# Kernel tuning notes

Measured on AMD Instinct MI355X. Metric: run time of the kernel, lower is better.

## Reference

```python
import jax, jax.numpy as jnp
import numpy as np

D_IN = 1024
N_HEADS = 16
DEPTH = D_IN // N_HEADS
SCALE = float(np.sqrt(DEPTH))


def setup_inputs() -> dict:
    key = jax.random.key(0)
    ks = jax.random.split(key, 11)
    B, S = 4, 1024
    s = 0.02
    return {
        "q": jax.random.normal(ks[0], (B, S, D_IN), jnp.float32),
        "k": jax.random.normal(ks[1], (B, S, D_IN), jnp.float32),
        "v": jax.random.normal(ks[2], (B, S, D_IN), jnp.float32),
        "mask": jnp.zeros((1, 1, S, S), jnp.float32),
        "wq_w": jax.random.normal(ks[3], (D_IN, D_IN), jnp.float32) * s,
        "wq_b": jax.random.normal(ks[4], (D_IN,), jnp.float32) * s,
        "wk_w": jax.random.normal(ks[5], (D_IN, D_IN), jnp.float32) * s,
        "wk_b": jax.random.normal(ks[6], (D_IN,), jnp.float32) * s,
        "wv_w": jax.random.normal(ks[7], (D_IN, D_IN), jnp.float32) * s,
        "wv_b": jax.random.normal(ks[8], (D_IN,), jnp.float32) * s,
        "pl_w": jax.random.normal(ks[9], (D_IN, D_IN), jnp.float32) * s,
        "pl_b": jax.random.normal(ks[10], (D_IN,), jnp.float32) * s,
    }


def _split_heads(x):
    # [B, S, D] -> [B, H, S, depth]
    B, S, _ = x.shape
    return x.reshape(B, S, N_HEADS, DEPTH).transpose(0, 2, 1, 3)


def reference(q, k, v, mask, wq_w, wq_b, wk_w, wk_b, wv_w, wv_b, pl_w, pl_b):
    # torch Linear: y = x @ W.T + b
    qh = _split_heads(q @ wq_w.T + wq_b)
    kh = _split_heads(k @ wk_w.T + wk_b)
    vh = _split_heads(v @ wv_w.T + wv_b)
    # [B, H, Sq, Sk]
    logits = jnp.einsum("bhqd,bhkd->bhqk", qh, kh) / SCALE
    logits = logits + mask * (-1e9)
    weights = jax.nn.softmax(logits, axis=-1)
    attn = jnp.einsum("bhqk,bhkd->bhqd", weights, vh)
    B = q.shape[0]
    attn = attn.transpose(0, 2, 1, 3).reshape(B, -1, D_IN)
    return attn @ pl_w.T + pl_b
```

## Files before the change

kernel.cpp:

```cpp
#include <hip/hip_runtime.h>
#include <stdint.h>

#define B_ 4
#define S_ 1024
#define DMODEL 1024
#define H_ 16
#define DP_ 64

typedef __attribute__((ext_vector_type(8))) short short8;
typedef __attribute__((ext_vector_type(4))) float floatx4;
typedef __attribute__((ext_vector_type(8))) unsigned short ushort8;
typedef __attribute__((ext_vector_type(4))) unsigned short ushort4v;

#define LOG2E 1.44269504088896f

__device__ __forceinline__ unsigned short f2bf(float x) {
    union { float f; unsigned int u; } c; c.f = x;
    unsigned int r = c.u + 0x7FFFu + ((c.u >> 16) & 1u);
    return (unsigned short)(r >> 16);
}
__device__ __forceinline__ unsigned short f2bf_fast(float x) {
    union { float f; unsigned int u; } c; c.f = x;
    return (unsigned short)((c.u + 0x8000u) >> 16);
}
__device__ __forceinline__ float bf2f(unsigned short b) {
    union { float f; unsigned int u; } c; c.u = ((unsigned int)b) << 16;
    return c.f;
}

#if __has_builtin(__builtin_amdgcn_exp2f)
#define EXP2(x) __builtin_amdgcn_exp2f(x)
#else
#define EXP2(x) exp2f(x)
#endif

#define GLDS16(gp, lp) __builtin_amdgcn_global_load_lds( \
    (const __attribute__((address_space(1))) void*)(gp),  \
    (__attribute__((address_space(3))) void*)(lp), 16, 0, 0)

__global__ __launch_bounds__(256) void convert_all(
    const float* __restrict__ q, const float* __restrict__ k, const float* __restrict__ v,
    const float* __restrict__ wq, const float* __restrict__ wk, const float* __restrict__ wv,
    const float* __restrict__ wp, const float* __restrict__ mask,
    unsigned short* __restrict__ ws)
{
    const unsigned g = blockIdx.x * 256u + threadIdx.x;
    const float* s; unsigned short* d; unsigned off; float sc = 1.0f;
    if (g < 524288u)        { s = q;  d = ws;            off = g; }
    else if (g < 1048576u)  { s = k;  d = ws + 4194304;  off = g - 524288u; }
    else if (g < 1572864u)  { s = v;  d = ws + 8388608;  off = g - 1048576u; }
    else if (g < 1703936u)  { s = wq; d = ws + 12582912; off = g - 1572864u; }
    else if (g < 1835008u)  { s = wk; d = ws + 13631488; off = g - 1703936u; }
    else if (g < 1966080u)  { s = wv; d = ws + 14680064; off = g - 1835008u; }
    else if (g < 2097152u)  { s = wp; d = ws + 15728640; off = g - 1966080u; }
    else { s = mask; d = ws + 16777216; off = g - 2097152u; sc = -1e9f * LOG2E; }
    const floatx4 a = ((const floatx4*)s)[(size_t)off * 2];
    const floatx4 b = ((const floatx4*)s)[(size_t)off * 2 + 1];
    ushort8 r;
    r[0] = f2bf(a[0] * sc); r[1] = f2bf(a[1] * sc); r[2] = f2bf(a[2] * sc); r[3] = f2bf(a[3] * sc);
    r[4] = f2bf(b[0] * sc); r[5] = f2bf(b[1] * sc); r[6] = f2bf(b[2] * sc); r[7] = f2bf(b[3] * sc);
    ((ushort8*)d)[off] = r;
}

template<bool SWAP>
__device__ __forceinline__ void gemm_body(
    const unsigned short* __restrict__ X, const unsigned short* __restrict__ W,
    const int row0, const int col0,
    unsigned short* Xs, unsigned short* Ws, floatx4* acc)
{
    const int tid = threadIdx.x, w = tid >> 6, lane = tid & 63;
    const int l15 = lane & 15, l4 = lane >> 4;
    const int wr = w >> 1, wc = w & 1;
    const int srow = lane >> 3;
    const int sgrp = (lane & 7) ^ srow;
    auto* XsL = (__attribute__((address_space(3))) unsigned short*)Xs;
    auto* WsL = (__attribute__((address_space(3))) unsigned short*)Ws;

    for (int it = 0; it < 16; it++) {
        const int kk = it * 64;
        __syncthreads();
        for (int j = 0; j < 4; j++) {
            const int rb = w * 32 + j * 8;
            GLDS16(X + (size_t)(row0 + rb + srow) * DMODEL + kk + sgrp * 8, XsL + rb * 64);
            GLDS16(W + (size_t)(col0 + rb + srow) * DMODEL + kk + sgrp * 8, WsL + rb * 64);
        }
        __syncthreads();
        for (int ks = 0; ks < 2; ks++) {
            const int slot = ((ks * 4 + l4) ^ (l15 & 7)) * 8;
            short8 xf[4], wf[4];
            for (int t = 0; t < 4; t++) {
                xf[t] = *(const short8*)(Xs + (wr * 64 + t * 16 + l15) * 64 + slot);
                wf[t] = *(const short8*)(Ws + (wc * 64 + t * 16 + l15) * 64 + slot);
            }
            for (int a = 0; a < 4; a++)
                for (int b2 = 0; b2 < 4; b2++)
                    acc[a * 4 + b2] = SWAP
                        ? __builtin_amdgcn_mfma_f32_16x16x32_bf16(wf[a], xf[b2], acc[a * 4 + b2], 0, 0, 0)
                        : __builtin_amdgcn_mfma_f32_16x16x32_bf16(xf[a], wf[b2], acc[a * 4 + b2], 0, 0, 0);
        }
    }
}

__global__ __launch_bounds__(256, 3) void qkv_gemm(
    const unsigned short* __restrict__ Xall, const unsigned short* __restrict__ Wall,
    const float* __restrict__ bq, const float* __restrict__ bk, const float* __restrict__ bv,
    unsigned short* __restrict__ Qh, unsigned short* __restrict__ Kh,
    unsigned short* __restrict__ Vt)
{
    __shared__ unsigned short Xs[8192];
    __shared__ unsigned short Ws[8192];
    const int sel = blockIdx.y >> 5;
    const int row0 = (blockIdx.y & 31) * 128, col0 = blockIdx.x * 128;
    const unsigned short* X = Xall + (size_t)sel * 4194304;
    const unsigned short* W = Wall + (size_t)sel * 1048576;
    const float* bias = (sel == 0) ? bq : (sel == 1) ? bk : bv;

    const int tid = threadIdx.x, w = tid >> 6, lane = tid & 63;
    const int l15 = lane & 15, l4 = lane >> 4;
    const int wr = w >> 1, wc = w & 1;

    floatx4 acc[16];
    for (int i = 0; i < 16; i++) acc[i] = (floatx4){0.f, 0.f, 0.f, 0.f};

    if (sel < 2) {
        gemm_body<true>(X, W, row0, col0, Xs, Ws, acc);
        unsigned short* Out = sel ? Kh : Qh;
        const float scale = sel ? 1.0f : 0.125f * LOG2E;
        for (int nt = 0; nt < 4; nt++) {
            const int n0 = col0 + wc * 64 + nt * 16 + l4 * 4;
            const floatx4 bv4 = *(const floatx4*)(bias + n0);
            const int h = n0 >> 6, d0 = n0 & 63;
            for (int mt = 0; mt < 4; mt++) {
                const int m = row0 + wr * 64 + mt * 16 + l15;
                const int b = m >> 10, s = m & 1023;
                const floatx4 a = acc[nt * 4 + mt];
                ushort4v pk;
                for (int i = 0; i < 4; i++) pk[i] = f2bf((a[i] + bv4[i]) * scale);
                *(ushort4v*)(Out + (((size_t)(b * H_ + h) * S_ + s) * DP_ + d0)) = pk;
            }
        }
    } else {
        gemm_body<false>(X, W, row0, col0, Xs, Ws, acc);
        for (int mt = 0; mt < 4; mt++) {
            const int m0 = row0 + wr * 64 + mt * 16 + l4 * 4;
            const int b = m0 >> 10, s0 = m0 & 1023;
            for (int nt = 0; nt < 4; nt++) {
                const int n = col0 + wc * 64 + nt * 16 + l15;
                const int h = n >> 6, d = n & 63;
                const float bvv = bias[n];
                const floatx4 a = acc[mt * 4 + nt];
                ushort4v pk;
                for (int i = 0; i < 4; i++) pk[i] = f2bf(a[i] + bvv);
                *(ushort4v*)(Vt + (((size_t)(b * H_ + h) * DP_ + d) * S_ + s0)) = pk;
            }
        }
    }
}

__global__ __launch_bounds__(256, 4) void out_gemm(
    const unsigned short* __restrict__ X, const unsigned short* __restrict__ W,
    const float* __restrict__ bias, float* __restrict__ Out)
{
    __shared__ unsigned short Xs[128 * 64];
    __shared__ unsigned short Ws[64 * 64];
    const int row0 = blockIdx.y * 128, col0 = blockIdx.x * 64;
    const int tid = threadIdx.x, w = tid >> 6, lane = tid & 63;
    const int l15 = lane & 15, l4 = lane >> 4;
    const int srow = lane >> 3, sgrp = (lane & 7) ^ srow;
    auto* XsL = (__attribute__((address_space(3))) unsigned short*)Xs;
    auto* WsL = (__attribute__((address_space(3))) unsigned short*)Ws;

    floatx4 acc[8];
    for (int i = 0; i < 8; i++) acc[i] = (floatx4){0.f, 0.f, 0.f, 0.f};

    for (int it = 0; it < 16; it++) {
        const int kk = it * 64;
        __syncthreads();
        for (int j = 0; j < 4; j++) {
            const int rb = w * 32 + j * 8;
            GLDS16(X + (size_t)(row0 + rb + srow) * DMODEL + kk + sgrp * 8, XsL + rb * 64);
        }
        for (int j = 0; j < 2; j++) {
            const int rb = w * 16 + j * 8;
            GLDS16(W + (size_t)(col0 + rb + srow) * DMODEL + kk + sgrp * 8, WsL + rb * 64);
        }
        __syncthreads();
        for (int ks = 0; ks < 2; ks++) {
            const int slot = ((ks * 4 + l4) ^ (l15 & 7)) * 8;
            short8 xf[2], wf[4];
            for (int t = 0; t < 2; t++)
                xf[t] = *(const short8*)(Xs + (w * 32 + t * 16 + l15) * 64 + slot);
            for (int t = 0; t < 4; t++)
                wf[t] = *(const short8*)(Ws + (t * 16 + l15) * 64 + slot);
            for (int nt = 0; nt < 4; nt++)
                for (int mt = 0; mt < 2; mt++)
                    acc[nt * 2 + mt] = __builtin_amdgcn_mfma_f32_16x16x32_bf16(
                        wf[nt], xf[mt], acc[nt * 2 + mt], 0, 0, 0);
        }
    }

    for (int nt = 0; nt < 4; nt++) {
        const int n0 = col0 + nt * 16 + l4 * 4;
        const floatx4 bv4 = *(const floatx4*)(bias + n0);
        for (int mt = 0; mt < 2; mt++) {
            const int m = row0 + w * 32 + mt * 16 + l15;
            floatx4 ov;
            for (int i = 0; i < 4; i++) ov[i] = acc[nt * 2 + mt][i] + bv4[i];
            *(floatx4*)(Out + (size_t)m * DMODEL + n0) = ov;
        }
    }
}

__global__ __launch_bounds__(256, 4) void attn_fwd(
    const unsigned short* __restrict__ Qh, const unsigned short* __restrict__ Kh,
    const unsigned short* __restrict__ Vt, const unsigned short* __restrict__ maskb,
    unsigned short* __restrict__ attnO)
{
    __shared__ unsigned short Ks[2 * 4096];
    __shared__ unsigned short Vs[2 * 4096];
    __shared__ unsigned short Ps[4 * 1024];
    auto* KsL = (__attribute__((address_space(3))) unsigned short*)Ks;
    auto* VsL = (__attribute__((address_space(3))) unsigned short*)Vs;

    const int bh = blockIdx.x, qt = blockIdx.y;
    const int b = bh >> 4, h = bh & 15;
    const int tid = threadIdx.x, w = tid >> 6, lane = tid & 63;
    const int l15 = lane & 15, l4 = lane >> 4;
    const int srow = lane >> 3, sgrp = (lane & 7) ^ srow;
    unsigned short* PsW = Ps + w * 1024;
    const int qg = qt * 64 + w * 16 + l15;

    short8 aq[2];
    for (int kd = 0; kd < 2; kd++)
        aq[kd] = *(const short8*)(Qh + ((size_t)bh * S_ + qg) * DP_ + kd * 32 + l4 * 8);

    for (int j = 0; j < 2; j++) {
        const int rb = w * 16 + j * 8;
        GLDS16(Kh + ((size_t)bh * S_ + rb + srow) * DP_ + sgrp * 8, KsL + rb * 64);
        GLDS16(Vt + ((size_t)bh * DP_ + rb + srow) * S_ + sgrp * 8, VsL + rb * 64);
    }
    ushort4v mk[4];
    for (int nt = 0; nt < 4; nt++)
        mk[nt] = *(const ushort4v*)(maskb + (size_t)qg * S_ + nt * 16 + l4 * 4);

    float l_i = 0.f;
    floatx4 o[4];
    for (int i = 0; i < 4; i++) o[i] = (floatx4){0.f, 0.f, 0.f, 0.f};

    for (int kt = 0; kt < 16; kt++) {
        const int cur = kt & 1, nxt = cur ^ 1;
        __syncthreads();
        ushort4v mkn[4];
        if (kt < 15) {
            for (int j = 0; j < 2; j++) {
                const int rb = w * 16 + j * 8;
                GLDS16(Kh + ((size_t)bh * S_ + (kt + 1) * 64 + rb + srow) * DP_ + sgrp * 8,
                       KsL + nxt * 4096 + rb * 64);
                GLDS16(Vt + ((size_t)bh * DP_ + rb + srow) * S_ + (kt + 1) * 64 + sgrp * 8,
                       VsL + nxt * 4096 + rb * 64);
            }
            for (int nt = 0; nt < 4; nt++)
                mkn[nt] = *(const ushort4v*)(maskb + (size_t)qg * S_ + (kt + 1) * 64 + nt * 16 + l4 * 4);
        }

        const unsigned short* Kc = Ks + cur * 4096;
        const unsigned short* Vc = Vs + cur * 4096;
        floatx4 sa[4];
        for (int nt = 0; nt < 4; nt++) sa[nt] = (floatx4){0.f, 0.f, 0.f, 0.f};
        for (int nt = 0; nt < 4; nt++)
            for (int kd = 0; kd < 2; kd++) {
                short8 ak = *(const short8*)(Kc + (nt * 16 + l15) * 64 + ((kd * 4 + l4) ^ (l15 & 7)) * 8);
                sa[nt] = __builtin_amdgcn_mfma_f32_16x16x32_bf16(ak, aq[kd], sa[nt], 0, 0, 0);
            }

        for (int nt = 0; nt < 4; nt++) {
            ushort4v pk;
            for (int i = 0; i < 4; i++) {
                const float p = EXP2(sa[nt][i] + bf2f(mk[nt][i]));
                l_i += p;
                pk[i] = f2bf_fast(p);
            }
            const int slot = ((nt * 2 + (l4 >> 1)) ^ (l15 & 7)) * 8 + (l4 & 1) * 4;
            *(ushort4v*)(PsW + l15 * 64 + slot) = pk;
        }

        short8 bp[2];
        for (int kc = 0; kc < 2; kc++)
            bp[kc] = *(const short8*)(PsW + l15 * 64 + (((kc * 4 + l4) ^ (l15 & 7)) * 8));
        for (int mt = 0; mt < 4; mt++)
            for (int kc = 0; kc < 2; kc++) {
                short8 av = *(const short8*)(Vc + (mt * 16 + l15) * 64 + ((kc * 4 + l4) ^ (l15 & 7)) * 8);
                o[mt] = __builtin_amdgcn_mfma_f32_16x16x32_bf16(av, bp[kc], o[mt], 0, 0, 0);
            }

        for (int nt = 0; nt < 4; nt++) mk[nt] = mkn[nt];
    }

    l_i += __shfl_xor(l_i, 16, 64);
    l_i += __shfl_xor(l_i, 32, 64);
    const float inv = 1.0f / l_i;

    for (int mt = 0; mt < 4; mt++) {
        ushort4v pk;
        for (int i = 0; i < 4; i++) pk[i] = f2bf(o[mt][i] * inv);
        const int slot = ((mt * 2 + (l4 >> 1)) ^ (l15 & 7)) * 8 + (l4 & 1) * 4;
        *(ushort4v*)(PsW + l15 * 64 + slot) = pk;
    }
    const int qr = lane >> 2;
    for (int t = 0; t < 2; t++) {
        const int gp = (lane & 3) * 2 + t;
        ushort8 ov = *(const ushort8*)(PsW + qr * 64 + ((gp ^ (qr & 7)) * 8));
        *(ushort8*)(attnO + ((size_t)(b * S_ + qt * 64 + w * 16 + qr)) * DMODEL + h * DP_ + gp * 8) = ov;
    }
}

extern "C" void kernel_launch(void* const* d_in, const int* in_sizes, int n_in,
                              void* d_out, int out_size, void* d_ws, size_t ws_size,
                              hipStream_t stream)
{
    (void)in_sizes; (void)n_in; (void)out_size; (void)ws_size;
    const float* q    = (const float*)d_in[0];
    const float* k    = (const float*)d_in[1];
    const float* v    = (const float*)d_in[2];
    const float* mask = (const float*)d_in[3];
    const float* wq_w = (const float*)d_in[4];
    const float* wq_b = (const float*)d_in[5];
    const float* wk_w = (const float*)d_in[6];
    const float* wk_b = (const float*)d_in[7];
    const float* wv_w = (const float*)d_in[8];
    const float* wv_b = (const float*)d_in[9];
    const float* pl_w = (const float*)d_in[10];
    const float* pl_b = (const float*)d_in[11];

    unsigned short* ws = (unsigned short*)d_ws;
    unsigned short* Xall  = ws;
    unsigned short* Wall  = ws + 12582912;
    unsigned short* Wp    = ws + 15728640;
    unsigned short* maskb = ws + 16777216;
    unsigned short* Qh    = ws + 17825792;
    unsigned short* Kh    = ws + 22020096;
    unsigned short* Vt    = ws + 4194304;
    unsigned short* attnB = ws;

    dim3 bb(256, 1, 1);
    convert_all<<<dim3(8704, 1, 1), bb, 0, stream>>>(q, k, v, wq_w, wk_w, wv_w, pl_w, mask, ws);
    qkv_gemm<<<dim3(8, 96, 1), bb, 0, stream>>>(Xall, Wall, wq_b, wk_b, wv_b, Qh, Kh, Vt);
    attn_fwd<<<dim3(64, 16, 1), bb, 0, stream>>>(Qh, Kh, Vt, maskb, attnB);
    out_gemm<<<dim3(16, 32, 1), bb, 0, stream>>>(attnB, Wp, pl_b, (float*)d_out);
}
```

Before: 226.2 us.

## Switch attention to 32x32x16 MFMA with 2x2 query/key wave split

Rewrites the attention kernel so each wave computes a 32-query by 32-key tile using 32x32x16 bf16 MFMA instead of four 16-row waves each using 16x16x32 MFMA. The waves split along query and key halves, share the P tile through LDS, and combine their partial softmax denominators through LDS at the end. The V prefetch is moved after an extra barrier so it can reuse buffer timing. The goal is fewer MFMA and LDS instructions per tile. In exchange it adds a second block-wide barrier per iteration and lowers the occupancy hint from 4 to 3 blocks per CU.

```diff
diff --git a/kernel.cpp b/kernel.cpp
--- a/kernel.cpp
+++ b/kernel.cpp
@@ -9,6 +9,7 @@
 
 typedef __attribute__((ext_vector_type(8))) short short8;
 typedef __attribute__((ext_vector_type(4))) float floatx4;
+typedef __attribute__((ext_vector_type(16))) float floatx16;
 typedef __attribute__((ext_vector_type(8))) unsigned short ushort8;
 typedef __attribute__((ext_vector_type(4))) unsigned short ushort4v;
 
@@ -211,106 +212,114 @@
     }
 }
 
-__global__ __launch_bounds__(256, 4) void attn_fwd(
+__global__ __launch_bounds__(256, 3) void attn_fwd(
     const unsigned short* __restrict__ Qh, const unsigned short* __restrict__ Kh,
     const unsigned short* __restrict__ Vt, const unsigned short* __restrict__ maskb,
     unsigned short* __restrict__ attnO)
 {
     __shared__ unsigned short Ks[2 * 4096];
     __shared__ unsigned short Vs[2 * 4096];
-    __shared__ unsigned short Ps[4 * 1024];
+    __shared__ unsigned short Ps[2 * 2048];
     auto* KsL = (__attribute__((address_space(3))) unsigned short*)Ks;
     auto* VsL = (__attribute__((address_space(3))) unsigned short*)Vs;
 
     const int bh = blockIdx.x, qt = blockIdx.y;
     const int b = bh >> 4, h = bh & 15;
     const int tid = threadIdx.x, w = tid >> 6, lane = tid & 63;
-    const int l15 = lane & 15, l4 = lane >> 4;
+    const int l31 = lane & 31, hh = lane >> 5;
+    const int qh = w >> 1, kh = w & 1;
     const int srow = lane >> 3, sgrp = (lane & 7) ^ srow;
-    unsigned short* PsW = Ps + w * 1024;
-    const int qg = qt * 64 + w * 16 + l15;
-
-    short8 aq[2];
-    for (int kd = 0; kd < 2; kd++)
-        aq[kd] = *(const short8*)(Qh + ((size_t)bh * S_ + qg) * DP_ + kd * 32 + l4 * 8);
+    unsigned short* PsQ = Ps + qh * 2048;
+    const int qg = qt * 64 + qh * 32 + l31;
+    const int sw7 = l31 & 7;
+
+    short8 bq[4];
+    for (int c = 0; c < 4; c++)
+        bq[c] = *(const short8*)(Qh + ((size_t)bh * S_ + qg) * DP_ + c * 16 + hh * 8);
 
     for (int j = 0; j < 2; j++) {
         const int rb = w * 16 + j * 8;
         GLDS16(Kh + ((size_t)bh * S_ + rb + srow) * DP_ + sgrp * 8, KsL + rb * 64);
         GLDS16(Vt + ((size_t)bh * DP_ + rb + srow) * S_ + sgrp * 8, VsL + rb * 64);
     }
-    ushort4v mk[4];
-    for (int nt = 0; nt < 4; nt++)
-        mk[nt] = *(const ushort4v*)(maskb + (size_t)qg * S_ + nt * 16 + l4 * 4);
+    ushort4v mk[4], mkn[4];
+    for (int rq = 0; rq < 4; rq++)
+        mk[rq] = *(const ushort4v*)(maskb + (size_t)qg * S_ + kh * 32 + rq * 8 + hh * 4);
 
     float l_i = 0.f;
-    floatx4 o[4];
-    for (int i = 0; i < 4; i++) o[i] = (floatx4){0.f, 0.f, 0.f, 0.f};
+    floatx16 o;
+    for (int i = 0; i < 16; i++) o[i] = 0.f;
 
     for (int kt = 0; kt < 16; kt++) {
         const int cur = kt & 1, nxt = cur ^ 1;
         __syncthreads();
-        ushort4v mkn[4];
         if (kt < 15) {
             for (int j = 0; j < 2; j++) {
                 const int rb = w * 16 + j * 8;
                 GLDS16(Kh + ((size_t)bh * S_ + (kt + 1) * 64 + rb + srow) * DP_ + sgrp * 8,
                        KsL + nxt * 4096 + rb * 64);
+            }
+            for (int rq = 0; rq < 4; rq++)
+                mkn[rq] = *(const ushort4v*)(maskb + (size_t)qg * S_ + (kt + 1) * 64 + kh * 32 + rq * 8 + hh * 4);
+        }
+
+        const unsigned short* Kc = Ks + cur * 4096;
+        floatx16 sa;
+        for (int i = 0; i < 16; i++) sa[i] = 0.f;
+        for (int c = 0; c < 4; c++) {
+            short8 ak = *(const short8*)(Kc + (kh * 32 + l31) * 64 + ((c * 2 + hh) ^ sw7) * 8);
+            sa = __builtin_amdgcn_mfma_f32_32x32x16_bf16(ak, bq[c], sa, 0, 0, 0);
+        }
+
+        for (int rq = 0; rq < 4; rq++) {
+            ushort4v pk;
+            for (int i = 0; i < 4; i++) {
+                const float p = EXP2(sa[rq * 4 + i] + bf2f(mk[rq][i]));
+                l_i += p;
+                pk[i] = f2bf_fast(p);
+            }
+            *(ushort4v*)(PsQ + l31 * 64 + ((kh * 4 + rq) ^ sw7) * 8 + hh * 4) = pk;
+        }
+        __syncthreads();
+        if (kt < 15) {
+            for (int j = 0; j < 2; j++) {
+                const int rb = w * 16 + j * 8;
                 GLDS16(Vt + ((size_t)bh * DP_ + rb + srow) * S_ + (kt + 1) * 64 + sgrp * 8,
                        VsL + nxt * 4096 + rb * 64);
             }
-            for (int nt = 0; nt < 4; nt++)
-                mkn[nt] = *(const ushort4v*)(maskb + (size_t)qg * S_ + (kt + 1) * 64 + nt * 16 + l4 * 4);
-        }
-
-        const unsigned short* Kc = Ks + cur * 4096;
+        }
+
         const unsigned short* Vc = Vs + cur * 4096;
-        floatx4 sa[4];
-        for (int nt = 0; nt < 4; nt++) sa[nt] = (floatx4){0.f, 0.f, 0.f, 0.f};
-        for (int nt = 0; nt < 4; nt++)
-            for (int kd = 0; kd < 2; kd++) {
-                short8 ak = *(const short8*)(Kc + (nt * 16 + l15) * 64 + ((kd * 4 + l4) ^ (l15 & 7)) * 8);
-                sa[nt] = __builtin_amdgcn_mfma_f32_16x16x32_bf16(ak, aq[kd], sa[nt], 0, 0, 0);
-            }
-
-        for (int nt = 0; nt < 4; nt++) {
-            ushort4v pk;
-            for (int i = 0; i < 4; i++) {
-                const float p = EXP2(sa[nt][i] + bf2f(mk[nt][i]));
-                l_i += p;
-                pk[i] = f2bf_fast(p);
-            }
-            const int slot = ((nt * 2 + (l4 >> 1)) ^ (l15 & 7)) * 8 + (l4 & 1) * 4;
-            *(ushort4v*)(PsW + l15 * 64 + slot) = pk;
-        }
-
-        short8 bp[2];
-        for (int kc = 0; kc < 2; kc++)
-            bp[kc] = *(const short8*)(PsW + l15 * 64 + (((kc * 4 + l4) ^ (l15 & 7)) * 8));
-        for (int mt = 0; mt < 4; mt++)
-            for (int kc = 0; kc < 2; kc++) {
-                short8 av = *(const short8*)(Vc + (mt * 16 + l15) * 64 + ((kc * 4 + l4) ^ (l15 & 7)) * 8);
-                o[mt] = __builtin_amdgcn_mfma_f32_16x16x32_bf16(av, bp[kc], o[mt], 0, 0, 0);
-            }
-
-        for (int nt = 0; nt < 4; nt++) mk[nt] = mkn[nt];
-    }
-
-    l_i += __shfl_xor(l_i, 16, 64);
+        for (int c2 = 0; c2 < 4; c2++) {
+            short8 av = *(const short8*)(Vc + (kh * 32 + l31) * 64 + ((c2 * 2 + hh) ^ sw7) * 8);
+            short8 bp = *(const short8*)(PsQ + l31 * 64 + ((c2 * 2 + hh) ^ sw7) * 8);
+            o = __builtin_amdgcn_mfma_f32_32x32x16_bf16(av, bp, o, 0, 0, 0);
+        }
+
+        if (kt < 15)
+            for (int rq = 0; rq < 4; rq++) mk[rq] = mkn[rq];
+    }
+
+    __syncthreads();
     l_i += __shfl_xor(l_i, 32, 64);
-    const float inv = 1.0f / l_i;
-
-    for (int mt = 0; mt < 4; mt++) {
+    float* Lbuf = (float*)Ks;
+    if (lane < 32) Lbuf[w * 32 + l31] = l_i;
+    __syncthreads();
+    const float inv = 1.0f / (Lbuf[qh * 64 + l31] + Lbuf[qh * 64 + 32 + l31]);
+
+    unsigned short* T = Ks + 1024;
+    for (int rq = 0; rq < 4; rq++) {
         ushort4v pk;
-        for (int i = 0; i < 4; i++) pk[i] = f2bf(o[mt][i] * inv);
-        const int slot = ((mt * 2 + (l4 >> 1)) ^ (l15 & 7)) * 8 + (l4 & 1) * 4;
-        *(ushort4v*)(PsW + l15 * 64 + slot) = pk;
-    }
-    const int qr = lane >> 2;
+        for (int i = 0; i < 4; i++) pk[i] = f2bf(o[rq * 4 + i] * inv);
+        const int qq = qh * 32 + l31;
+        *(ushort4v*)(T + qq * 64 + ((kh * 4 + rq) ^ sw7) * 8 + hh * 4) = pk;
+    }
+    __syncthreads();
+    const int r = tid >> 2;
     for (int t = 0; t < 2; t++) {
-        const int gp = (lane & 3) * 2 + t;
-        ushort8 ov = *(const ushort8*)(PsW + qr * 64 + ((gp ^ (qr & 7)) * 8));
-        *(ushort8*)(attnO + ((size_t)(b * S_ + qt * 64 + w * 16 + qr)) * DMODEL + h * DP_ + gp * 8) = ov;
+        const int g = (tid & 3) + t * 4;
+        ushort8 ov = *(const ushort8*)(T + r * 64 + ((g ^ (r & 7)) * 8));
+        *(ushort8*)(attnO + ((size_t)(b * S_ + qt * 64 + r)) * DMODEL + h * DP_ + g * 8) = ov;
     }
 }
 
```

Measured after the change: 220.1 us. 1.03x faster.

## Process 32 query rows per wave in attention and stage GEMM output through LDS

Applied to the files above, without the earlier changes.

The attention kernel now has each wave handle two 16-row query groups, so every K and V tile loaded into shared memory is reused across 128 queries per block, which halves the grid and the K/V traffic. Launch bounds drop to 2 blocks per CU to make room for the larger register footprint, and the output is written through a shared-memory transpose so global stores are coalesced. The output GEMM epilogue likewise stages fp32 results through swizzled LDS before writing full rows. The trade-offs are lower occupancy and extra barriers.

```diff
diff --git a/kernel.cpp b/kernel.cpp
--- a/kernel.cpp
+++ b/kernel.cpp
@@ -199,26 +199,39 @@
         }
     }
 
-    for (int nt = 0; nt < 4; nt++) {
-        const int n0 = col0 + nt * 16 + l4 * 4;
-        const floatx4 bv4 = *(const floatx4*)(bias + n0);
-        for (int mt = 0; mt < 2; mt++) {
-            const int m = row0 + w * 32 + mt * 16 + l15;
-            floatx4 ov;
-            for (int i = 0; i < 4; i++) ov[i] = acc[nt * 2 + mt][i] + bv4[i];
-            *(floatx4*)(Out + (size_t)m * DMODEL + n0) = ov;
-        }
-    }
-}
-
-__global__ __launch_bounds__(256, 4) void attn_fwd(
+    float* Cb = (float*)Xs;
+    for (int c = 0; c < 2; c++) {
+        __syncthreads();
+        if ((w >> 1) == c) {
+            for (int nt = 0; nt < 4; nt++) {
+                const int n0 = col0 + nt * 16 + l4 * 4;
+                const floatx4 bv4 = *(const floatx4*)(bias + n0);
+                for (int mt = 0; mt < 2; mt++) {
+                    const int ml = (w & 1) * 32 + mt * 16 + l15;
+                    floatx4 ov;
+                    for (int i = 0; i < 4; i++) ov[i] = acc[nt * 2 + mt][i] + bv4[i];
+                    *(floatx4*)(Cb + ml * 64 + ((nt * 4 + l4) ^ l15) * 4) = ov;
+                }
+            }
+        }
+        __syncthreads();
+        for (int rnd = 0; rnd < 4; rnd++) {
+            const int r = (tid >> 4) + rnd * 16;
+            const int gs = tid & 15;
+            floatx4 v = *(const floatx4*)(Cb + r * 64 + ((gs ^ (r & 15)) * 4));
+            *(floatx4*)(Out + (size_t)(row0 + c * 64 + r) * DMODEL + col0 + gs * 4) = v;
+        }
+    }
+}
+
+__global__ __launch_bounds__(256, 2) void attn_fwd(
     const unsigned short* __restrict__ Qh, const unsigned short* __restrict__ Kh,
     const unsigned short* __restrict__ Vt, const unsigned short* __restrict__ maskb,
     unsigned short* __restrict__ attnO)
 {
     __shared__ unsigned short Ks[2 * 4096];
     __shared__ unsigned short Vs[2 * 4096];
-    __shared__ unsigned short Ps[4 * 1024];
+    __shared__ unsigned short Ps[4 * 2048];
     auto* KsL = (__attribute__((address_space(3))) unsigned short*)Ks;
     auto* VsL = (__attribute__((address_space(3))) unsigned short*)Vs;
 
@@ -227,30 +240,36 @@
     const int tid = threadIdx.x, w = tid >> 6, lane = tid & 63;
     const int l15 = lane & 15, l4 = lane >> 4;
     const int srow = lane >> 3, sgrp = (lane & 7) ^ srow;
-    unsigned short* PsW = Ps + w * 1024;
-    const int qg = qt * 64 + w * 16 + l15;
-
-    short8 aq[2];
-    for (int kd = 0; kd < 2; kd++)
-        aq[kd] = *(const short8*)(Qh + ((size_t)bh * S_ + qg) * DP_ + kd * 32 + l4 * 8);
+    const int sw7 = l15 & 7;
+    unsigned short* PsW = Ps + w * 2048;
+    const int q0 = qt * 128 + w * 32;
+    const int qa = q0 + l15, qb = q0 + 16 + l15;
+
+    short8 aq[2][2];
+    for (int kd = 0; kd < 2; kd++) {
+        aq[0][kd] = *(const short8*)(Qh + ((size_t)bh * S_ + qa) * DP_ + kd * 32 + l4 * 8);
+        aq[1][kd] = *(const short8*)(Qh + ((size_t)bh * S_ + qb) * DP_ + kd * 32 + l4 * 8);
+    }
 
     for (int j = 0; j < 2; j++) {
         const int rb = w * 16 + j * 8;
         GLDS16(Kh + ((size_t)bh * S_ + rb + srow) * DP_ + sgrp * 8, KsL + rb * 64);
         GLDS16(Vt + ((size_t)bh * DP_ + rb + srow) * S_ + sgrp * 8, VsL + rb * 64);
     }
-    ushort4v mk[4];
-    for (int nt = 0; nt < 4; nt++)
-        mk[nt] = *(const ushort4v*)(maskb + (size_t)qg * S_ + nt * 16 + l4 * 4);
-
-    float l_i = 0.f;
-    floatx4 o[4];
-    for (int i = 0; i < 4; i++) o[i] = (floatx4){0.f, 0.f, 0.f, 0.f};
+    ushort4v mk[2][4], mkn[2][4];
+    for (int nt = 0; nt < 4; nt++) {
+        mk[0][nt] = *(const ushort4v*)(maskb + (size_t)qa * S_ + nt * 16 + l4 * 4);
+        mk[1][nt] = *(const ushort4v*)(maskb + (size_t)qb * S_ + nt * 16 + l4 * 4);
+    }
+
+    float l_i[2] = {0.f, 0.f};
+    floatx4 o[2][4];
+    for (int qg = 0; qg < 2; qg++)
+        for (int i = 0; i < 4; i++) o[qg][i] = (floatx4){0.f, 0.f, 0.f, 0.f};
 
     for (int kt = 0; kt < 16; kt++) {
         const int cur = kt & 1, nxt = cur ^ 1;
         __syncthreads();
-        ushort4v mkn[4];
         if (kt < 15) {
             for (int j = 0; j < 2; j++) {
                 const int rb = w * 16 + j * 8;
@@ -259,58 +278,73 @@
                 GLDS16(Vt + ((size_t)bh * DP_ + rb + srow) * S_ + (kt + 1) * 64 + sgrp * 8,
                        VsL + nxt * 4096 + rb * 64);
             }
-            for (int nt = 0; nt < 4; nt++)
-                mkn[nt] = *(const ushort4v*)(maskb + (size_t)qg * S_ + (kt + 1) * 64 + nt * 16 + l4 * 4);
+            for (int nt = 0; nt < 4; nt++) {
+                mkn[0][nt] = *(const ushort4v*)(maskb + (size_t)qa * S_ + (kt + 1) * 64 + nt * 16 + l4 * 4);
+                mkn[1][nt] = *(const ushort4v*)(maskb + (size_t)qb * S_ + (kt + 1) * 64 + nt * 16 + l4 * 4);
+            }
         }
 
         const unsigned short* Kc = Ks + cur * 4096;
         const unsigned short* Vc = Vs + cur * 4096;
-        floatx4 sa[4];
-        for (int nt = 0; nt < 4; nt++) sa[nt] = (floatx4){0.f, 0.f, 0.f, 0.f};
+        floatx4 sa[2][4];
+        for (int qg = 0; qg < 2; qg++)
+            for (int nt = 0; nt < 4; nt++) sa[qg][nt] = (floatx4){0.f, 0.f, 0.f, 0.f};
         for (int nt = 0; nt < 4; nt++)
             for (int kd = 0; kd < 2; kd++) {
-                short8 ak = *(const short8*)(Kc + (nt * 16 + l15) * 64 + ((kd * 4 + l4) ^ (l15 & 7)) * 8);
-                sa[nt] = __builtin_amdgcn_mfma_f32_16x16x32_bf16(ak, aq[kd], sa[nt], 0, 0, 0);
-            }
-
-        for (int nt = 0; nt < 4; nt++) {
-            ushort4v pk;
-            for (int i = 0; i < 4; i++) {
-                const float p = EXP2(sa[nt][i] + bf2f(mk[nt][i]));
-                l_i += p;
-                pk[i] = f2bf_fast(p);
-            }
-            const int slot = ((nt * 2 + (l4 >> 1)) ^ (l15 & 7)) * 8 + (l4 & 1) * 4;
-            *(ushort4v*)(PsW + l15 * 64 + slot) = pk;
-        }
-
-        short8 bp[2];
-        for (int kc = 0; kc < 2; kc++)
-            bp[kc] = *(const short8*)(PsW + l15 * 64 + (((kc * 4 + l4) ^ (l15 & 7)) * 8));
+                short8 ak = *(const short8*)(Kc + (nt * 16 + l15) * 64 + ((kd * 4 + l4) ^ sw7) * 8);
+                sa[0][nt] = __builtin_amdgcn_mfma_f32_16x16x32_bf16(ak, aq[0][kd], sa[0][nt], 0, 0, 0);
+                sa[1][nt] = __builtin_amdgcn_mfma_f32_16x16x32_bf16(ak, aq[1][kd], sa[1][nt], 0, 0, 0);
+            }
+
+        for (int qg = 0; qg < 2; qg++)
+            for (int nt = 0; nt < 4; nt++) {
+                ushort4v pk;
+                for (int i = 0; i < 4; i++) {
+                    const float p = EXP2(sa[qg][nt][i] + bf2f(mk[qg][nt][i]));
+                    l_i[qg] += p;
+                    pk[i] = f2bf_fast(p);
+                }
+                const int slot = ((nt * 2 + (l4 >> 1)) ^ sw7) * 8 + (l4 & 1) * 4;
+                *(ushort4v*)(PsW + (qg * 16 + l15) * 64 + slot) = pk;
+            }
+
+        short8 bp[2][2];
+        for (int qg = 0; qg < 2; qg++)
+            for (int kc = 0; kc < 2; kc++)
+                bp[qg][kc] = *(const short8*)(PsW + (qg * 16 + l15) * 64 + (((kc * 4 + l4) ^ sw7) * 8));
         for (int mt = 0; mt < 4; mt++)
             for (int kc = 0; kc < 2; kc++) {
-                short8 av = *(const short8*)(Vc + (mt * 16 + l15) * 64 + ((kc * 4 + l4) ^ (l15 & 7)) * 8);
-                o[mt] = __builtin_amdgcn_mfma_f32_16x16x32_bf16(av, bp[kc], o[mt], 0, 0, 0);
-            }
-
-        for (int nt = 0; nt < 4; nt++) mk[nt] = mkn[nt];
-    }
-
-    l_i += __shfl_xor(l_i, 16, 64);
-    l_i += __shfl_xor(l_i, 32, 64);
-    const float inv = 1.0f / l_i;
-
-    for (int mt = 0; mt < 4; mt++) {
-        ushort4v pk;
-        for (int i = 0; i < 4; i++) pk[i] = f2bf(o[mt][i] * inv);
-        const int slot = ((mt * 2 + (l4 >> 1)) ^ (l15 & 7)) * 8 + (l4 & 1) * 4;
-        *(ushort4v*)(PsW + l15 * 64 + slot) = pk;
-    }
-    const int qr = lane >> 2;
-    for (int t = 0; t < 2; t++) {
-        const int gp = (lane & 3) * 2 + t;
-        ushort8 ov = *(const ushort8*)(PsW + qr * 64 + ((gp ^ (qr & 7)) * 8));
-        *(ushort8*)(attnO + ((size_t)(b * S_ + qt * 64 + w * 16 + qr)) * DMODEL + h * DP_ + gp * 8) = ov;
+                short8 av = *(const short8*)(Vc + (mt * 16 + l15) * 64 + ((kc * 4 + l4) ^ sw7) * 8);
+                o[0][mt] = __builtin_amdgcn_mfma_f32_16x16x32_bf16(av, bp[0][kc], o[0][mt], 0, 0, 0);
+                o[1][mt] = __builtin_amdgcn_mfma_f32_16x16x32_bf16(av, bp[1][kc], o[1][mt], 0, 0, 0);
+            }
+
+        if (kt < 15)
+            for (int qg = 0; qg < 2; qg++)
+                for (int nt = 0; nt < 4; nt++) mk[qg][nt] = mkn[qg][nt];
+    }
+
+    __syncthreads();
+    float inv[2];
+    for (int qg = 0; qg < 2; qg++) {
+        l_i[qg] += __shfl_xor(l_i[qg], 16, 64);
+        l_i[qg] += __shfl_xor(l_i[qg], 32, 64);
+        inv[qg] = 1.0f / l_i[qg];
+    }
+    unsigned short* T = Ks;
+    for (int qg = 0; qg < 2; qg++)
+        for (int mt = 0; mt < 4; mt++) {
+            ushort4v pk;
+            for (int i = 0; i < 4; i++) pk[i] = f2bf(o[qg][mt][i] * inv[qg]);
+            const int slot = ((mt * 2 + (l4 >> 1)) ^ sw7) * 8 + (l4 & 1) * 4;
+            *(ushort4v*)(T + (w * 32 + qg * 16 + l15) * 64 + slot) = pk;
+        }
+    __syncthreads();
+    const int r = tid >> 1;
+    for (int rnd = 0; rnd < 4; rnd++) {
+        const int g = (tid & 1) * 4 + rnd;
+        ushort8 ov = *(const ushort8*)(T + r * 64 + ((g ^ (r & 7)) * 8));
+        *(ushort8*)(attnO + ((size_t)(b * S_ + qt * 128 + r)) * DMODEL + h * DP_ + g * 8) = ov;
     }
 }
 
@@ -345,6 +379,6 @@
     dim3 bb(256, 1, 1);
     convert_all<<<dim3(8704, 1, 1), bb, 0, stream>>>(q, k, v, wq_w, wk_w, wv_w, pl_w, mask, ws);
     qkv_gemm<<<dim3(8, 96, 1), bb, 0, stream>>>(Xall, Wall, wq_b, wk_b, wv_b, Qh, Kh, Vt);
-    attn_fwd<<<dim3(64, 16, 1), bb, 0, stream>>>(Qh, Kh, Vt, maskb, attnB);
+    attn_fwd<<<dim3(64, 8, 1), bb, 0, stream>>>(Qh, Kh, Vt, maskb, attnB);
     out_gemm<<<dim3(16, 32, 1), bb, 0, stream>>>(attnB, Wp, pl_b, (float*)d_out);
 }
```

Result: no change. 227.0 us (+0.4%).
